# Optimization experiments

Measured on AMD Instinct MI355X. Metric: run time of the kernel, lower is better.

The kernel has to match this reference:

```python
import jax, jax.numpy as jnp
import numpy as np

B, N, D = 4, 16384, 1024
RANK, NUM_Q = 16, 8
SPARSITY = 0.1
K = max(1, int(N * SPARSITY))  # 1638


def setup_inputs() -> dict:
    key = jax.random.key(0)
    k1, k2, k3 = jax.random.split(key, 3)
    x = jax.random.normal(k1, (B, N, D), dtype=jnp.float32)
    Wk = jax.random.normal(k2, (RANK, D), dtype=jnp.float32)
    queries = jax.random.normal(k3, (NUM_Q, RANK), dtype=jnp.float32)
    return {"x": x, "Wk": Wk, "queries": queries}


def reference(x, Wk, queries):
    # k_proj: [b, n, d] @ [d, rank] -> [b, n, rank]
    keys = jnp.einsum("bnd,rd->bnr", x, Wk)
    # scores: [q, r] x [b, n, r] -> [b, q, n]
    scores = jnp.einsum("qr,bnr->bqn", queries, keys)
    # max over queries -> [b, n]
    token_scores = scores.max(axis=1)
    # eval mode: no jitter noise
    _, indices = jax.lax.top_k(token_scores, K)  # [b, K]
    indices = jnp.sort(indices, axis=-1)
    return indices
```

## Files before the change

kernel.cpp:

```cpp
#include <hip/hip_runtime.h>
#include <stdint.h>

#define B_ 4
#define N_ 16384
#define D_ 1024
#define RANK_ 16
#define NUMQ_ 8
#define KSEL_ 1638

__global__ __launch_bounds__(256) void wq_kernel(const float* __restrict__ Wk,
                                                 const float* __restrict__ queries,
                                                 float* __restrict__ Wq) {
    int i = blockIdx.x * 256 + threadIdx.x;
    if (i >= NUMQ_ * D_) return;
    int q = i >> 10;
    int d = i & (D_ - 1);
    float acc = 0.f;
#pragma unroll
    for (int r = 0; r < RANK_; ++r)
        acc += queries[q * RANK_ + r] * Wk[r * D_ + d];
    Wq[i] = acc;
}

#define TOK 4

#define FOLD(dst, a, b, bit, dist)                          \
    {                                                       \
        float _send = (bit) ? (a) : (b);                    \
        float _recv = __shfl_xor(_send, (dist), 64);        \
        (dst) = ((bit) ? (b) : (a)) + _recv;                \
    }

__global__ __launch_bounds__(256) void score_kernel(const float* __restrict__ x,
                                                    const float* __restrict__ Wq,
                                                    unsigned int* __restrict__ keys) {
    __shared__ float sWq[NUMQ_ * D_];
    for (int i = threadIdx.x; i < (NUMQ_ * D_) / 4; i += 256)
        ((float4*)sWq)[i] = ((const float4*)Wq)[i];
    __syncthreads();

    const int lane = threadIdx.x & 63;
    const int wave = threadIdx.x >> 6;
    const int gw = blockIdx.x * 4 + wave;
    const int numWaves = gridDim.x * 4;
    const int totalTok = B_ * N_;

    const int l5 = (lane >> 5) & 1;
    const int l4 = (lane >> 4) & 1;
    const int l3 = (lane >> 3) & 1;

    for (int t0 = gw * TOK; t0 < totalTok; t0 += numWaves * TOK) {
        float acc[TOK][NUMQ_];
#pragma unroll
        for (int t = 0; t < TOK; ++t)
#pragma unroll
            for (int q = 0; q < NUMQ_; ++q) acc[t][q] = 0.f;

#pragma unroll
        for (int j = 0; j < 4; ++j) {
            const int off = j * 256 + lane * 4;
            float4 xv[TOK];
#pragma unroll
            for (int t = 0; t < TOK; ++t)
                xv[t] = *(const float4*)(x + (size_t)(t0 + t) * D_ + off);
#pragma unroll
            for (int q = 0; q < NUMQ_; ++q) {
                float4 w = *(const float4*)(sWq + q * D_ + off);
#pragma unroll
                for (int t = 0; t < TOK; ++t) {
                    acc[t][q] += xv[t].x * w.x;
                    acc[t][q] += xv[t].y * w.y;
                    acc[t][q] += xv[t].z * w.z;
                    acc[t][q] += xv[t].w * w.w;
                }
            }
        }

#pragma unroll
        for (int t = 0; t < TOK; ++t) {
            float n0, n1, n2, n3;
            FOLD(n0, acc[t][0], acc[t][4], l5, 32)
            FOLD(n1, acc[t][1], acc[t][5], l5, 32)
            FOLD(n2, acc[t][2], acc[t][6], l5, 32)
            FOLD(n3, acc[t][3], acc[t][7], l5, 32)
            float m0, m1;
            FOLD(m0, n0, n2, l4, 16)
            FOLD(m1, n1, n3, l4, 16)
            float p;
            FOLD(p, m0, m1, l3, 8)
            p += __shfl_xor(p, 4, 64);
            p += __shfl_xor(p, 2, 64);
            p += __shfl_xor(p, 1, 64);
            float mx = p;
            mx = fmaxf(mx, __shfl_xor(mx, 8, 64));
            mx = fmaxf(mx, __shfl_xor(mx, 16, 64));
            mx = fmaxf(mx, __shfl_xor(mx, 32, 64));
            if (lane == t) {
                unsigned int u = __float_as_uint(mx);
                u = (u & 0x80000000u) ? ~u : (u | 0x80000000u);
                keys[t0 + t] = u;
            }
        }
    }
}

__global__ __launch_bounds__(1024) void topk_kernel(const unsigned int* __restrict__ keys,
                                                    int* __restrict__ out) {
    __shared__ __align__(16) unsigned int sKeys[N_];
    __shared__ unsigned int hist[2048];
    __shared__ unsigned int sSuf[1024];
    __shared__ unsigned int waveTot[16];
    __shared__ unsigned int wTotG[16];
    __shared__ int sTs;
    __shared__ unsigned int sPrefix, sR;

    const int b = blockIdx.x;
    const int tid = threadIdx.x;
    const int lane = tid & 63;
    const int wave = tid >> 6;

    const uint4* kv = (const uint4*)(keys + b * N_);
    uint4* sk4 = (uint4*)sKeys;
    for (int i = tid; i < N_ / 4; i += 1024) sk4[i] = kv[i];
    __syncthreads();

    unsigned int prefix = 0;
    unsigned int R = KSEL_;

    const int shifts[3] = {21, 10, 0};
    const int widths[3] = {11, 11, 10};

#pragma unroll 1
    for (int pass = 0; pass < 3; ++pass) {
        const int shift = shifts[pass];
        const unsigned int nb = 1u << widths[pass];
        const unsigned int binmask = nb - 1u;
        const unsigned int maskHi = (pass == 0) ? 0u
                                  : (0xFFFFFFFFu << (shift + widths[pass]));

        for (int i = tid; i < (int)nb; i += 1024) hist[i] = 0;
        __syncthreads();
        for (int i = tid; i < N_ / 4; i += 1024) {
            uint4 u4 = sk4[i];
            unsigned int us[4] = {u4.x, u4.y, u4.z, u4.w};
#pragma unroll
            for (int c = 0; c < 4; ++c) {
                unsigned int u = us[c];
                if ((u & maskHi) == prefix)
                    atomicAdd(&hist[(u >> shift) & binmask], 1u);
            }
        }
        __syncthreads();

        const int seg = (int)(nb >> 10);
        unsigned int v = 0;
        for (int j = 0; j < seg; ++j) v += hist[tid * seg + j];

#pragma unroll
        for (int d = 1; d < 64; d <<= 1) {
            unsigned int t = __shfl_down(v, (unsigned)d, 64);
            if (lane + d < 64) v += t;
        }
        if (lane == 0) waveTot[wave] = v;
        __syncthreads();
        unsigned int basev = 0;
        for (int w = wave + 1; w < 16; ++w) basev += waveTot[w];
        unsigned int suf = v + basev;
        sSuf[tid] = suf;
        __syncthreads();

        if (suf >= R && (tid == 1023 || sSuf[tid + 1] < R)) sTs = tid;
        __syncthreads();
        const int ts = sTs;

        if (tid == 0) {
            unsigned int cum = (ts < 1023) ? sSuf[ts + 1] : 0u;
            int sel = ts * seg;
            for (int bin = ts * seg + seg - 1; bin >= ts * seg; --bin) {
                unsigned int c = hist[bin];
                if (cum + c >= R) { sel = bin; break; }
                cum += c;
            }
            sPrefix = prefix | ((unsigned int)sel << shift);
            sR = R - cum;
        }
        __syncthreads();
        prefix = sPrefix;
        R = sR;
        __syncthreads();
    }

    const unsigned int T = prefix;
    const unsigned int need = R;

    const int CHUNK = N_ / 1024;
    const int base = tid * CHUNK;
    unsigned int cGT = 0, cEQ = 0;
    for (int i = 0; i < CHUNK / 4; ++i) {
        uint4 u4 = sk4[(base >> 2) + i];
        cGT += (u4.x > T) + (u4.y > T) + (u4.z > T) + (u4.w > T);
        cEQ += (u4.x == T) + (u4.y == T) + (u4.z == T) + (u4.w == T);
    }
    unsigned int packed = (cGT << 16) | cEQ;
    unsigned int pv = packed;
#pragma unroll
    for (int d = 1; d < 64; d <<= 1) {
        unsigned int t = __shfl_up(pv, (unsigned)d, 64);
        if (lane >= d) pv += t;
    }
    if (lane == 63) wTotG[wave] = pv;
    __syncthreads();
    unsigned int pbase = 0;
    for (int w = 0; w < wave; ++w) pbase += wTotG[w];
    unsigned int excl = pbase + pv - packed;
    unsigned int gt = excl >> 16;
    unsigned int eq = excl & 0xFFFFu;

    int* ob = out + b * KSEL_;
    for (int i = 0; i < CHUNK; ++i) {
        unsigned int u = sKeys[base + i];
        if (u > T) {
            unsigned int eqSel = (eq < need) ? eq : need;
            ob[gt + eqSel] = base + i;
            gt++;
        } else if (u == T) {
            if (eq < need) ob[gt + eq] = base + i;
            eq++;
        }
    }
}

extern "C" void kernel_launch(void* const* d_in, const int* in_sizes, int n_in,
                              void* d_out, int out_size, void* d_ws, size_t ws_size,
                              hipStream_t stream) {
    const float* x       = (const float*)d_in[0];
    const float* Wk      = (const float*)d_in[1];
    const float* queries = (const float*)d_in[2];
    int* out = (int*)d_out;

    float*        Wq   = (float*)d_ws;
    unsigned int* keys = (unsigned int*)((char*)d_ws + 32 * 1024);

    wq_kernel<<<(NUMQ_ * D_ + 255) / 256, 256, 0, stream>>>(Wk, queries, Wq);
    score_kernel<<<2048, 256, 0, stream>>>(x, Wq, keys);
    topk_kernel<<<B_, 1024, 0, stream>>>(keys, out);
}
```

Baseline: 376.8 us.

## Fuse Wq computation into score kernel and histogram during top-k key load

Drops the separate wq_kernel launch: each score block now computes the query-projected weights Wq directly from Wk and queries into shared memory. The top-k kernel builds the first radix histogram pass while copying keys into shared memory, which removes one full scan of the keys. The score grid is halved to 1024 blocks, which cuts the redundant per-block Wq work but means fewer waves to spread the x stream across.

Measured after the change: 375.0 us. No clear change (-0.5%).

```diff
diff --git a/kernel.cpp b/kernel.cpp
--- a/kernel.cpp
+++ b/kernel.cpp
@@ -8,20 +8,6 @@
 #define NUMQ_ 8
 #define KSEL_ 1638
 
-__global__ __launch_bounds__(256) void wq_kernel(const float* __restrict__ Wk,
-                                                 const float* __restrict__ queries,
-                                                 float* __restrict__ Wq) {
-    int i = blockIdx.x * 256 + threadIdx.x;
-    if (i >= NUMQ_ * D_) return;
-    int q = i >> 10;
-    int d = i & (D_ - 1);
-    float acc = 0.f;
-#pragma unroll
-    for (int r = 0; r < RANK_; ++r)
-        acc += queries[q * RANK_ + r] * Wk[r * D_ + d];
-    Wq[i] = acc;
-}
-
 #define TOK 4
 
 #define FOLD(dst, a, b, bit, dist)                          \
@@ -32,11 +18,32 @@
     }
 
 __global__ __launch_bounds__(256) void score_kernel(const float* __restrict__ x,
-                                                    const float* __restrict__ Wq,
+                                                    const float* __restrict__ Wk,
+                                                    const float* __restrict__ queries,
                                                     unsigned int* __restrict__ keys) {
     __shared__ float sWq[NUMQ_ * D_];
-    for (int i = threadIdx.x; i < (NUMQ_ * D_) / 4; i += 256)
-        ((float4*)sWq)[i] = ((const float4*)Wq)[i];
+
+    {
+        const int d0 = threadIdx.x * 4;
+        float4 acc[NUMQ_];
+#pragma unroll
+        for (int q = 0; q < NUMQ_; ++q) acc[q] = make_float4(0.f, 0.f, 0.f, 0.f);
+#pragma unroll
+        for (int r = 0; r < RANK_; ++r) {
+            float4 wk = *(const float4*)(Wk + r * D_ + d0);
+#pragma unroll
+            for (int q = 0; q < NUMQ_; ++q) {
+                float qv = queries[q * RANK_ + r];
+                acc[q].x += qv * wk.x;
+                acc[q].y += qv * wk.y;
+                acc[q].z += qv * wk.z;
+                acc[q].w += qv * wk.w;
+            }
+        }
+#pragma unroll
+        for (int q = 0; q < NUMQ_; ++q)
+            *(float4*)(sWq + q * D_ + d0) = acc[q];
+    }
     __syncthreads();
 
     const int lane = threadIdx.x & 63;
@@ -119,9 +126,19 @@
     const int lane = tid & 63;
     const int wave = tid >> 6;
 
+    for (int i = tid; i < 2048; i += 1024) hist[i] = 0;
+    __syncthreads();
+
     const uint4* kv = (const uint4*)(keys + b * N_);
     uint4* sk4 = (uint4*)sKeys;
-    for (int i = tid; i < N_ / 4; i += 1024) sk4[i] = kv[i];
+    for (int i = tid; i < N_ / 4; i += 1024) {
+        uint4 u4 = kv[i];
+        sk4[i] = u4;
+        atomicAdd(&hist[u4.x >> 21], 1u);
+        atomicAdd(&hist[u4.y >> 21], 1u);
+        atomicAdd(&hist[u4.z >> 21], 1u);
+        atomicAdd(&hist[u4.w >> 21], 1u);
+    }
     __syncthreads();
 
     unsigned int prefix = 0;
@@ -135,22 +152,23 @@
         const int shift = shifts[pass];
         const unsigned int nb = 1u << widths[pass];
         const unsigned int binmask = nb - 1u;
-        const unsigned int maskHi = (pass == 0) ? 0u
-                                  : (0xFFFFFFFFu << (shift + widths[pass]));
-
-        for (int i = tid; i < (int)nb; i += 1024) hist[i] = 0;
-        __syncthreads();
-        for (int i = tid; i < N_ / 4; i += 1024) {
-            uint4 u4 = sk4[i];
-            unsigned int us[4] = {u4.x, u4.y, u4.z, u4.w};
-#pragma unroll
-            for (int c = 0; c < 4; ++c) {
-                unsigned int u = us[c];
-                if ((u & maskHi) == prefix)
-                    atomicAdd(&hist[(u >> shift) & binmask], 1u);
-            }
-        }
-        __syncthreads();
+
+        if (pass > 0) {
+            const unsigned int maskHi = 0xFFFFFFFFu << (shift + widths[pass]);
+            for (int i = tid; i < (int)nb; i += 1024) hist[i] = 0;
+            __syncthreads();
+            for (int i = tid; i < N_ / 4; i += 1024) {
+                uint4 u4 = sk4[i];
+                unsigned int us[4] = {u4.x, u4.y, u4.z, u4.w};
+#pragma unroll
+                for (int c = 0; c < 4; ++c) {
+                    unsigned int u = us[c];
+                    if ((u & maskHi) == prefix)
+                        atomicAdd(&hist[(u >> shift) & binmask], 1u);
+                }
+            }
+            __syncthreads();
+        }
 
         const int seg = (int)(nb >> 10);
         unsigned int v = 0;
@@ -238,10 +256,8 @@
     const float* queries = (const float*)d_in[2];
     int* out = (int*)d_out;
 
-    float*        Wq   = (float*)d_ws;
-    unsigned int* keys = (unsigned int*)((char*)d_ws + 32 * 1024);
-
-    wq_kernel<<<(NUMQ_ * D_ + 255) / 256, 256, 0, stream>>>(Wk, queries, Wq);
-    score_kernel<<<2048, 256, 0, stream>>>(x, Wq, keys);
+    unsigned int* keys = (unsigned int*)d_ws;
+
+    score_kernel<<<1024, 256, 0, stream>>>(x, Wk, queries, keys);
     topk_kernel<<<B_, 1024, 0, stream>>>(keys, out);
 }
```
